# Optimization experiments

Measured on AMD Instinct MI355X. Metric: run time of the kernel, lower is better.

The kernel has to match this reference:

```python
import jax, jax.numpy as jnp
import numpy as np
from jax import lax

# dims from the TED skeleton used by speech2affective_gestures
N, T, J, C = 256, 1024, 9, 3      # batch, frames, directed edges (graph1 nodes), coords
K1, K2 = 5, 3                     # spatial partitions of A1, A2
F1, F2 = 16, 16                   # st_gcn output channels
NUM_PARTS, MAX_EDGES = 3, 3       # body parts, edges per part
BODY_PARTS = np.array([[0, 1, 2], [3, 4, 5], [6, 7, 8]])  # body_parts_edge_idx
EPS = 1e-5
LEAK = 0.01


def conv2d_nchw(x, w):
    kh = w.shape[2]
    return lax.conv_general_dilated(x, w, (1, 1), ((kh // 2, kh // 2), (0, 0)),
                                    dimension_numbers=("NCHW", "OIHW", "NCHW"))


def conv1d_nch(x, w):
    k = w.shape[2]
    return lax.conv_general_dilated(x, w, (1,), ((k // 2, k // 2),),
                                    dimension_numbers=("NCH", "OIH", "NCH"))


def bn1d(x, w, b, m, v):
    # inference-mode BatchNorm1d over channel axis 1 of (N, C, T)
    scale = w / jnp.sqrt(v + EPS)
    return x * scale[None, :, None] + (b - m * scale)[None, :, None]


def leaky(x):
    return jnp.where(x > 0, x, LEAK * x)


def setup_inputs() -> dict:
    key = jax.random.key(0)
    ks = jax.random.split(key, 12)
    s = 0.05
    return {
        "poses": jax.random.normal(ks[0], (N, T, J * C), jnp.float32),
        "A1": jax.random.uniform(ks[1], (K1, J, J), jnp.float32) / J,
        "A2": jax.random.uniform(ks[2], (K2, NUM_PARTS, NUM_PARTS), jnp.float32) / NUM_PARTS,
        "W1": jax.random.normal(ks[3], (F1 * K1, C, 9, 1), jnp.float32) * s,
        "b1": jnp.zeros((F1 * K1,), jnp.float32),
        "W2": jax.random.normal(ks[4], (F2 * K2, MAX_EDGES * F1, 9, 1), jnp.float32) * s,
        "b2": jnp.zeros((F2 * K2,), jnp.float32),
        "Wc1": jax.random.normal(ks[5], (16, F2 * NUM_PARTS, 5), jnp.float32) * s,
        "bc1": jnp.zeros((16,), jnp.float32),
        "bn1_w": jnp.ones((16,), jnp.float32), "bn1_b": jnp.zeros((16,), jnp.float32),
        "bn1_m": jnp.zeros((16,), jnp.float32), "bn1_v": jnp.ones((16,), jnp.float32),
        "Wc2": jax.random.normal(ks[6], (8, 16, 3), jnp.float32) * s,
        "bc2": jnp.zeros((8,), jnp.float32),
        "bn2_w": jnp.ones((8,), jnp.float32), "bn2_b": jnp.zeros((8,), jnp.float32),
        "bn2_m": jnp.zeros((8,), jnp.float32), "bn2_v": jnp.ones((8,), jnp.float32),
    }


def reference(poses, A1, A2, W1, b1, W2, b2, Wc1, bc1, bn1_w, bn1_b, bn1_m, bn1_v,
              Wc2, bc2, bn2_w, bn2_b, bn2_m, bn2_v):
    n, t, jc = poses.shape
    x = jnp.transpose(poses.reshape(n, t, J, C), (0, 3, 1, 2))  # (n, 3, t, 9)

    # st_gcn1: temporal conv -> split K partitions -> graph contraction with A1
    y = conv2d_nchw(x, W1) + b1[None, :, None, None]            # (n, K1*F1, t, 9)
    y = y.reshape(n, K1, F1, t, J)
    feat1 = jnp.einsum("nkctv,kvw->nctw", y, A1)                # (n, 16, t, 9)

    # body-part gather/pack: feat2_in channel layout is (c slow, edge fast)
    g = feat1[:, :, :, BODY_PARTS]                              # (n, 16, t, parts, edges)
    feat2_in = jnp.transpose(g, (0, 1, 4, 2, 3)).reshape(n, F1 * MAX_EDGES, t, NUM_PARTS)

    # st_gcn2
    y2 = conv2d_nchw(feat2_in, W2) + b2[None, :, None, None]    # (n, K2*F2, t, 3)
    y2 = y2.reshape(n, K2, F2, t, NUM_PARTS)
    feat2 = jnp.einsum("nkctv,kvw->nctw", y2, A2)               # (n, 16, t, 3)

    # flatten (c, v) with c slow -> (n, 48, t)
    feat3_in = jnp.transpose(feat2, (0, 1, 3, 2)).reshape(n, F2 * NUM_PARTS, t)

    h = leaky(bn1d(conv1d_nch(feat3_in, Wc1) + bc1[None, :, None], bn1_w, bn1_b, bn1_m, bn1_v))
    h = leaky(bn1d(conv1d_nch(h, Wc2) + bc2[None, :, None], bn2_w, bn2_b, bn2_m, bn2_v))
    return jnp.transpose(h, (0, 2, 1))                          # (n, t, 8)
```

## Files before the change

kernel.cpp:

```cpp
#include <hip/hip_runtime.h>

namespace {
constexpr int T_ = 1024;
constexpr int NBATCH = 256;

constexpr int WFB_OFF    = 0;
constexpr int WFC_OFF    = 82944;
constexpr int WFD_OFF    = 221184;
constexpr int WBIG_OFF   = 231424;
constexpr int WFE_OFF    = 252928;
constexpr int BIASB_OFF  = 254976;
constexpr int BIASC_OFF  = 255552;
constexpr int BIASD_OFF  = 255744;
constexpr int BIASBIG_OFF= 255808;
constexpr int BIASE_OFF  = 255872;

constexpr int R0 = 41472;
constexpr int R1 = R0 + 69120;
constexpr int R2 = R1 + 5120;
constexpr int R3 = R2 + 1024;
constexpr int R4 = R3 + 29952;
constexpr int R5 = R4 + 144;
constexpr int R6 = R5 + 48;
constexpr int R7 = R6 + 16;
constexpr int R8 = R7 + 8;

constexpr int SLAB_OFF  = 0;
constexpr int H1_OFF    = 18688;
constexpr int WBIGS_OFF = 27392;
constexpr int WFES_OFF  = 48896;
constexpr int SMEM_MAIN = 50944;
static_assert(SMEM_MAIN * 3 <= 163840, "3 blocks/CU");

constexpr int TT_FX     = 50;
constexpr int FXF2IN    = 0;
constexpr int FXF3      = FXF2IN + 72 * 320;
constexpr int FXSLAB    = FXF3 + 68 * 144;
constexpr int FXH1      = FXSLAB;
constexpr int SMEM_FX   = FXSLAB + 72 * 80;
static_assert(SMEM_FX <= 65536, "fixup LDS");

typedef __attribute__((ext_vector_type(8))) short short8v;
typedef __attribute__((ext_vector_type(4))) float f32x4;

__device__ inline unsigned short f2b(float f) {
  union { float f; unsigned u; } v; v.f = f;
  unsigned r = (v.u + 0x7FFFu + ((v.u >> 16) & 1u)) >> 16;
  return (unsigned short)r;
}
__device__ inline float b2f(unsigned short u) {
  union { unsigned u; float f; } v; v.u = ((unsigned)u) << 16;
  return v.f;
}
__device__ inline int fx_f2in_byte(int row, int slot, int within) {
  return FXF2IN + row * 320 + ((slot ^ ((row >> 2) & 3)) << 4) + within;
}
}

__global__ __launch_bounds__(256) void prep1_kernel(
    const float* __restrict__ A1, const float* __restrict__ A2,
    const float* __restrict__ W1, const float* __restrict__ b1,
    const float* __restrict__ W2, const float* __restrict__ b2,
    const float* __restrict__ Wc1, const float* __restrict__ bc1,
    const float* __restrict__ bn1w, const float* __restrict__ bn1b,
    const float* __restrict__ bn1m, const float* __restrict__ bn1v,
    const float* __restrict__ Wc2, const float* __restrict__ bc2,
    const float* __restrict__ bn2w, const float* __restrict__ bn2b,
    const float* __restrict__ bn2m, const float* __restrict__ bn2v,
    unsigned char* __restrict__ ws, float* __restrict__ wcomp) {
  unsigned short* wfB = (unsigned short*)(ws + WFB_OFF);
  unsigned short* wfC = (unsigned short*)(ws + WFC_OFF);
  unsigned short* wfD = (unsigned short*)(ws + WFD_OFF);
  unsigned short* wfE = (unsigned short*)(ws + WFE_OFF);
  float* biasB = (float*)(ws + BIASB_OFF);
  float* biasC = (float*)(ws + BIASC_OFF);
  float* biasD = (float*)(ws + BIASD_OFF);
  float* biasE = (float*)(ws + BIASE_OFF);
  for (int idx = blockIdx.x * 256 + threadIdx.x; idx < R8; idx += gridDim.x * 256) {
    if (idx < R0) {
      int ncol = idx / 288, k = idx - ncol * 288;
      int dh = k >> 5, mm = k & 31;
      float val = 0.f;
      if (mm < 27) {
        int v = mm / 3, ci = mm - v * 3;
        int p = ncol / 48, rr = ncol - p * 48, c = rr / 3, e = rr - c * 3;
        int w = p * 3 + e;
        for (int k5 = 0; k5 < 5; ++k5)
          val += W1[(k5 * 16 + c) * 27 + ci * 9 + dh] * A1[k5 * 81 + v * 9 + w];
      }
      wfB[idx] = f2b(val);
    } else if (idx < R1) {
      int i2 = idx - R0;
      int nc = i2 / 1440, k = i2 - nc * 1440;
      int dh = k / 160, off = k - dh * 160;
      float val = 0.f;
      if (off < 144) {
        int p = off / 48, ci2 = off - p * 48;
        int c2 = nc / 3, w2 = nc - c2 * 3;
        for (int k2 = 0; k2 < 3; ++k2)
          val += W2[(k2 * 16 + c2) * 432 + ci2 * 9 + dh] * A2[k2 * 9 + p * 3 + w2];
      }
      wfC[i2] = f2b(val);
    } else if (idx < R2) {
      int i3 = idx - R1;
      int o3 = i3 / 320, k = i3 - o3 * 320;
      int d = k >> 6, nc = k & 63;
      float val = 0.f;
      if (nc < 48) {
        float s1 = bn1w[o3] * rsqrtf(bn1v[o3] + 1e-5f);
        val = Wc1[o3 * 240 + nc * 5 + d] * s1;
      }
      wfD[i3] = f2b(val);
    } else if (idx < R3) {
      int i4 = idx - R2;
      int o4 = i4 >> 6, k = i4 & 63;
      float val = 0.f;
      if (o4 < 8 && k < 48) {
        int d = k >> 4, ci = k & 15;
        float s2 = bn2w[o4] * rsqrtf(bn2v[o4] + 1e-5f);
        val = Wc2[(o4 * 16 + ci) * 3 + d] * s2;
      }
      wfE[i4] = f2b(val);
    } else if (idx < R4) {
      int i5 = idx - R3;
      int o3 = i5 / 1872, rem = i5 - o3 * 1872;
      int dh2 = rem / 144, ncol = rem - dh2 * 144;
      int p = ncol / 48, ci2 = ncol - p * 48;
      float s1 = bn1w[o3] * rsqrtf(bn1v[o3] + 1e-5f);
      float acc = 0.f;
      for (int d = 0; d < 5; ++d) {
        int dh = dh2 - d;
        if (dh < 0 || dh > 8) continue;
        float wd = 0.f;
        for (int nc = 0; nc < 48; ++nc) {
          int c2 = nc / 3, w2 = nc - c2 * 3;
          float wc = 0.f;
          for (int k2 = 0; k2 < 3; ++k2)
            wc += W2[(k2 * 16 + c2) * 432 + ci2 * 9 + dh] * A2[k2 * 9 + p * 3 + w2];
          wd += Wc1[o3 * 240 + nc * 5 + d] * wc;
        }
        acc += wd * s1;
      }
      wcomp[i5] = acc;
    } else if (idx < R5) {
      int ib = idx - R4;
      int p = ib / 48, rr = ib - p * 48, c = rr / 3, e = rr - c * 3;
      int w = p * 3 + e;
      float val = 0.f;
      for (int k5 = 0; k5 < 5; ++k5)
        for (int v = 0; v < 9; ++v)
          val += b1[k5 * 16 + c] * A1[k5 * 81 + v * 9 + w];
      biasB[ib] = val;
    } else if (idx < R6) {
      int nc = idx - R5, c2 = nc / 3, w2 = nc - c2 * 3;
      float val = 0.f;
      for (int k2 = 0; k2 < 3; ++k2)
        for (int p = 0; p < 3; ++p)
          val += b2[k2 * 16 + c2] * A2[k2 * 9 + p * 3 + w2];
      biasC[nc] = val;
    } else if (idx < R7) {
      int o3 = idx - R6;
      float s1 = bn1w[o3] * rsqrtf(bn1v[o3] + 1e-5f);
      biasD[o3] = bc1[o3] * s1 + bn1b[o3] - bn1m[o3] * s1;
    } else {
      int o4 = idx - R7;
      float s2 = bn2w[o4] * rsqrtf(bn2v[o4] + 1e-5f);
      biasE[o4] = bc2[o4] * s2 + bn2b[o4] - bn2m[o4] * s2;
    }
  }
}

__global__ __launch_bounds__(256) void prep2_kernel(
    const float* __restrict__ Wc1, const float* __restrict__ bn1w,
    const float* __restrict__ bn1v, const float* __restrict__ wcomp,
    unsigned char* __restrict__ ws) {
  __shared__ float stgf[48 * 288];
  __shared__ float wl[1872];
  __shared__ float pr[256];
  __shared__ float pbias[192];
  const int dt = blockIdx.x, o3 = blockIdx.y;
  const int tid = threadIdx.x;
  const int m1 = tid & 31, p = tid >> 5;
  const unsigned short* wfB = (const unsigned short*)(ws + WFB_OFF);
  unsigned short* wBIG = (unsigned short*)(ws + WBIG_OFF);

  for (int i = tid; i < 1872; i += 256) wl[i] = wcomp[o3 * 1872 + i];

  const int lo = (dt - 8) > 0 ? (dt - 8) : 0;
  const int hi = (dt < 12) ? dt : 12;
  float acc = 0.f;
  for (int c = 0; c < 3; ++c) {
    __syncthreads();
    for (int i = tid; i < 48 * 288; i += 256)
      stgf[i] = b2f(wfB[c * 13824 + i]);
    __syncthreads();
    for (int dh2 = lo; dh2 <= hi; ++dh2) {
      const int dh1 = dt - dh2;
      const float* wr = wl + dh2 * 144 + c * 48 + p * 6;
      const float* br = stgf + (p * 6) * 288 + dh1 * 32 + m1;
#pragma unroll
      for (int j = 0; j < 6; ++j)
        acc += wr[j] * br[j * 288];
    }
  }
  pr[tid] = acc;
  __syncthreads();
  if (tid < 32) {
    float s = pr[tid];
#pragma unroll
    for (int pp = 1; pp < 8; ++pp) s += pr[pp * 32 + tid];
    wBIG[o3 * 672 + dt * 32 + tid] = f2b(s);
  }
  if (dt == 0) {
    if (tid < 144) {
      float s = 0.f;
      for (int dh2 = 0; dh2 < 13; ++dh2) s += wl[dh2 * 144 + tid];
      pbias[tid] = s * ((const float*)(ws + BIASB_OFF))[tid];
    } else if (tid < 192) {
      int nc = tid - 144;
      float s1 = bn1w[o3] * rsqrtf(bn1v[o3] + 1e-5f);
      float s = 0.f;
#pragma unroll
      for (int d = 0; d < 5; ++d) s += Wc1[o3 * 240 + nc * 5 + d];
      pbias[tid] = s * s1 * ((const float*)(ws + BIASC_OFF))[nc];
    }
    __syncthreads();
    if (tid == 0) {
      float accb = ((const float*)(ws + BIASD_OFF))[o3];
      for (int i = 0; i < 192; ++i) accb += pbias[i];
      ((float*)(ws + BIASBIG_OFF))[o3] = accb;
    }
  }
}

__global__ __launch_bounds__(256, 3) void main_kernel(
    const float* __restrict__ poses, const unsigned char* __restrict__ ws,
    float* __restrict__ out) {
  __shared__ __attribute__((aligned(16))) unsigned char smem[SMEM_MAIN];
  const int tid = threadIdx.x;
  const int n = blockIdx.y;
  const int t0 = blockIdx.x * 256;
  const int w = tid >> 6, l = tid & 63, lrow = l & 15, q = l >> 4, q8 = q * 8;

  {
    unsigned* s32 = (unsigned*)(smem + SLAB_OFF);
    for (int idx = tid; idx < 292 * 16; idx += 256) {
      int r = idx >> 4, mi = idx & 15, m0 = mi * 2;
      int t = t0 - 18 + r;
      float v0 = 0.f, v1 = 0.f;
      if (t >= 0 && t < T_) {
        const float* src = poses + ((long)n * T_ + t) * 27;
        if (m0 < 27) v0 = src[m0];
        if (m0 + 1 < 27) v1 = src[m0 + 1];
      }
      s32[idx] = (unsigned)f2b(v0) | ((unsigned)f2b(v1) << 16);
    }
    const unsigned* wbg = (const unsigned*)(ws + WBIG_OFF);
    unsigned* d1 = (unsigned*)(smem + WBIGS_OFF);
    for (int idx = tid; idx < 5376; idx += 256) d1[idx] = wbg[idx];
    const unsigned* wfe = (const unsigned*)(ws + WFE_OFF);
    unsigned* d2 = (unsigned*)(smem + WFES_OFF);
    for (int idx = tid; idx < 512; idx += 256) d2[idx] = wfe[idx];
  }
  __syncthreads();

  const float bb = ((const float*)(ws + BIASBIG_OFF))[lrow];
  const float be = ((const float*)(ws + BIASE_OFF))[lrow & 7];

  short8v B[21];
#pragma unroll
  for (int dt = 0; dt < 21; ++dt)
    B[dt] = *(const short8v*)(smem + WBIGS_OFF + lrow * 1344 + dt * 64 + q8 * 2);

#pragma unroll
  for (int i = 0; i < 5; ++i) {
    if (i == 4 && w != 0) continue;
    const int mt = (i < 4) ? (w + i * 4) : 16;
    const int sbase = SLAB_OFF + (mt * 16 + lrow) * 64 + q8 * 2;
    f32x4 c0 = {0.f, 0.f, 0.f, 0.f}, c1 = {0.f, 0.f, 0.f, 0.f};
    short8v a[7];
#pragma unroll
    for (int dt = 0; dt < 7; ++dt) a[dt] = *(const short8v*)(smem + sbase + dt * 64);
#pragma unroll
    for (int dt = 0; dt < 7; ++dt) {
      if (dt & 1) c1 = __builtin_amdgcn_mfma_f32_16x16x32_bf16(a[dt], B[dt], c1, 0, 0, 0);
      else        c0 = __builtin_amdgcn_mfma_f32_16x16x32_bf16(a[dt], B[dt], c0, 0, 0, 0);
    }
#pragma unroll
    for (int dt = 0; dt < 7; ++dt) a[dt] = *(const short8v*)(smem + sbase + (7 + dt) * 64);
#pragma unroll
    for (int dt = 0; dt < 7; ++dt) {
      if (dt & 1) c1 = __builtin_amdgcn_mfma_f32_16x16x32_bf16(a[dt], B[7 + dt], c1, 0, 0, 0);
      else        c0 = __builtin_amdgcn_mfma_f32_16x16x32_bf16(a[dt], B[7 + dt], c0, 0, 0, 0);
    }
#pragma unroll
    for (int dt = 0; dt < 7; ++dt) a[dt] = *(const short8v*)(smem + sbase + (14 + dt) * 64);
#pragma unroll
    for (int dt = 0; dt < 7; ++dt) {
      if (dt & 1) c1 = __builtin_amdgcn_mfma_f32_16x16x32_bf16(a[dt], B[14 + dt], c1, 0, 0, 0);
      else        c0 = __builtin_amdgcn_mfma_f32_16x16x32_bf16(a[dt], B[14 + dt], c0, 0, 0, 0);
    }
    const int hbase = H1_OFF + (mt * 16 + q * 4) * 32 + lrow * 2;
#pragma unroll
    for (int jj = 0; jj < 4; ++jj) {
      float x = c0[jj] + c1[jj] + bb;
      float h = x > 0.f ? x : 0.01f * x;
      *(unsigned short*)(smem + hbase + jj * 32) = f2b(h);
    }
  }
  __syncthreads();

  const short8v E0 = *(const short8v*)(smem + WFES_OFF + lrow * 128 + q8 * 2);
  const short8v E1 = *(const short8v*)(smem + WFES_OFF + lrow * 128 + 64 + q8 * 2);
#pragma unroll
  for (int i = 0; i < 4; ++i) {
    const int mte = w + i * 4;
    const int abase = H1_OFF + (7 + mte * 16 + lrow) * 32 + q8 * 2;
    short8v A0v = *(const short8v*)(smem + abase);
    short8v A1v = *(const short8v*)(smem + abase + 64);
    f32x4 acc = {0.f, 0.f, 0.f, 0.f};
    acc = __builtin_amdgcn_mfma_f32_16x16x32_bf16(A0v, E0, acc, 0, 0, 0);
    acc = __builtin_amdgcn_mfma_f32_16x16x32_bf16(A1v, E1, acc, 0, 0, 0);
    if (lrow < 8) {
      const long ob = ((long)n * T_ + t0 + mte * 16 + q * 4) * 8 + lrow;
#pragma unroll
      for (int jj = 0; jj < 4; ++jj) {
        float x = acc[jj] + be;
        out[ob + jj * 8] = x > 0.f ? x : 0.01f * x;
      }
    }
  }
}

__global__ __launch_bounds__(256, 4) void fixup_kernel(
    const float* __restrict__ poses,
    const float* __restrict__ Wc2, const float* __restrict__ bc2,
    const float* __restrict__ bn2w, const float* __restrict__ bn2b,
    const float* __restrict__ bn2m, const float* __restrict__ bn2v,
    const unsigned char* __restrict__ ws, float* __restrict__ out) {
  __shared__ __attribute__((aligned(16))) unsigned char smem[SMEM_FX];
  const unsigned short* wfB = (const unsigned short*)(ws + WFB_OFF);
  const unsigned short* wfC = (const unsigned short*)(ws + WFC_OFF);
  const unsigned short* wfD = (const unsigned short*)(ws + WFD_OFF);
  const float* biasB = (const float*)(ws + BIASB_OFF);
  const float* biasC = (const float*)(ws + BIASC_OFF);
  const float* biasD = (const float*)(ws + BIASD_OFF);

  const int tid = threadIdx.x;
  const int n = blockIdx.y;
  const int e = blockIdx.x;
  const int t0 = e ? (T_ - TT_FX) : 0;
  const int w = tid >> 6;
  const int l = tid & 63;
  const int lrow = l & 15;
  const int q = l >> 4;
  const int q8 = q * 8;

  {
    unsigned* slab32 = (unsigned*)(smem + FXSLAB);
    for (int it = tid; it < 72 * 20; it += 256) {
      int r = it / 20, mi = it - r * 20;
      int t = t0 - 11 + r;
      int m0 = mi * 2;
      float v0 = 0.f, v1 = 0.f;
      if (t >= 0 && t < T_) {
        const float* src = poses + ((long)n * T_ + t) * 27;
        if (m0 < 27) v0 = src[m0];
        if (m0 + 1 < 27) v1 = src[m0 + 1];
      }
      slab32[it] = (unsigned)f2b(v0) | ((unsigned)f2b(v1) << 16);
    }
    for (int it = tid; it < 64 * 8; it += 256) {
      int r = it >> 3, u = it & 7;
      int s = 18 + (u >> 2);
      *(unsigned*)(smem + fx_f2in_byte(r, s, (u & 3) * 4)) = 0;
    }
    for (int it = tid; it < 8 * 80; it += 256) {
      int r = 64 + it / 80, u = it - (it / 80) * 80;
      *(unsigned*)(smem + FXF2IN + r * 320 + u * 4) = 0;
    }
    for (int it = tid; it < 68 * 8 + 12 * 24; it += 256) {
      if (it < 68 * 8) {
        int r = it >> 3, u = it & 7;
        *(unsigned*)(smem + FXF3 + r * 144 + 96 + u * 4) = 0;
      } else {
        int k2 = it - 68 * 8;
        int r = 56 + k2 / 24, u = k2 - (k2 / 24) * 24;
        *(unsigned*)(smem + FXF3 + r * 144 + u * 4) = 0;
      }
    }
  }
  __syncthreads();

  {
    const int ntS = (w == 0) ? 0 : (2 * w + 1);
    const int ntN = (w == 0) ? 3 : 2;
#pragma unroll
    for (int ni = 0; ni < 3; ++ni) {
      if (ni < ntN) {
        const int nt = ntS + ni;
        short8v b[9];
#pragma unroll
        for (int dh = 0; dh < 9; ++dh)
          b[dh] = *(const short8v*)(wfB + (nt * 16 + lrow) * 288 + dh * 32 + q8);
        const int ncol = nt * 16 + lrow;
        const float bias = biasB[ncol];
#pragma unroll
        for (int mt = 0; mt < 4; ++mt) {
          short8v a[9];
#pragma unroll
          for (int dh = 0; dh < 9; ++dh)
            a[dh] = *(const short8v*)(smem + FXSLAB + ((mt * 16 + lrow + dh) * 40 + q8) * 2);
          f32x4 c0 = {0.f, 0.f, 0.f, 0.f}, c1 = {0.f, 0.f, 0.f, 0.f};
#pragma unroll
          for (int dh = 0; dh < 9; ++dh) {
            if (dh & 1) c1 = __builtin_amdgcn_mfma_f32_16x16x32_bf16(a[dh], b[dh], c1, 0, 0, 0);
            else        c0 = __builtin_amdgcn_mfma_f32_16x16x32_bf16(a[dh], b[dh], c0, 0, 0, 0);
          }
#pragma unroll
          for (int jj = 0; jj < 4; ++jj) {
            const int r = mt * 16 + q * 4 + jj;
            const int t = t0 - 7 + r;
            float v = (t >= 0 && t < T_) ? c0[jj] + c1[jj] + bias : 0.f;
            *(unsigned short*)(smem + fx_f2in_byte(r, ncol >> 3, (ncol & 7) * 2)) = f2b(v);
          }
        }
      }
    }
  }
  __syncthreads();

  if (w < 3) {
    const int nt = w;
    const int ncol2 = nt * 16 + lrow;
    const float bias = biasC[ncol2];
    f32x4 acc[4];
#pragma unroll
    for (int mt = 0; mt < 4; ++mt) acc[mt] = {0.f, 0.f, 0.f, 0.f};
#pragma unroll
    for (int g = 0; g < 5; ++g) {
      short8v b[9];
#pragma unroll
      for (int i = 0; i < 9; ++i) {
        const int kf = g * 9 + i, dh = kf / 5, kkl = kf % 5;
        b[i] = *(const short8v*)(wfC + ncol2 * 1440 + dh * 160 + kkl * 32 + q8);
      }
#pragma unroll
      for (int mt = 0; mt < 4; ++mt) {
        short8v a[9];
#pragma unroll
        for (int i = 0; i < 9; ++i) {
          const int kf = g * 9 + i, dh = kf / 5, kkl = kf % 5;
          a[i] = *(const short8v*)(smem + fx_f2in_byte(mt * 16 + lrow + dh, 4 * kkl + q, 0));
        }
#pragma unroll
        for (int i = 0; i < 9; ++i)
          acc[mt] = __builtin_amdgcn_mfma_f32_16x16x32_bf16(a[i], b[i], acc[mt], 0, 0, 0);
      }
    }
#pragma unroll
    for (int mt = 0; mt < 4; ++mt) {
#pragma unroll
      for (int jj = 0; jj < 4; ++jj) {
        const int rt3 = mt * 16 + q * 4 + jj;
        if (rt3 < 56) {
          const int t = t0 - 3 + rt3;
          float v = (t >= 0 && t < T_) ? acc[mt][jj] + bias : 0.f;
          *(unsigned short*)(smem + FXF3 + rt3 * 144 + ncol2 * 2) = f2b(v);
        }
      }
    }
  }
  __syncthreads();

  {
    const int arow = w * 16 + lrow;
    short8v a[10], b[10];
#pragma unroll
    for (int kf = 0; kf < 10; ++kf) {
      const int d = kf >> 1, kkl = kf & 1;
      b[kf] = *(const short8v*)(wfD + lrow * 320 + d * 64 + kkl * 32 + q8);
      a[kf] = *(const short8v*)(smem + FXF3 + (arow + d) * 144 + (kkl * 32 + q8) * 2);
    }
    f32x4 c0 = {0.f, 0.f, 0.f, 0.f}, c1 = {0.f, 0.f, 0.f, 0.f};
#pragma unroll
    for (int kf = 0; kf < 10; ++kf) {
      if (kf & 1) c1 = __builtin_amdgcn_mfma_f32_16x16x32_bf16(a[kf], b[kf], c1, 0, 0, 0);
      else        c0 = __builtin_amdgcn_mfma_f32_16x16x32_bf16(a[kf], b[kf], c0, 0, 0, 0);
    }
    const float bias = biasD[lrow];
#pragma unroll
    for (int jj = 0; jj < 4; ++jj) {
      const int rh = w * 16 + q * 4 + jj;
      if (rh < 52) {
        const int t = t0 - 1 + rh;
        float v = 0.f;
        if (t >= 0 && t < T_) {
          float x = c0[jj] + c1[jj] + bias;
          v = x > 0.f ? x : 0.01f * x;
        }
        *(float*)(smem + FXH1 + (rh * 17 + lrow) * 4) = v;
      }
    }
  }
  __syncthreads();

  for (int it = tid; it < TT_FX * 8; it += 256) {
    int rt = it >> 3, o4 = it & 7;
    int t = t0 + rt;
    if (t >= T_) continue;
    if (e ? (t < 1017) : (t >= 7)) continue;
    float s2 = bn2w[o4] * rsqrtf(bn2v[o4] + 1e-5f);
    float t2 = bc2[o4] * s2 + bn2b[o4] - bn2m[o4] * s2;
    float acc = 0.f;
#pragma unroll
    for (int d = 0; d < 3; ++d) {
      const float* hr = (const float*)(smem + FXH1 + (rt + d) * 68);
#pragma unroll
      for (int ci = 0; ci < 16; ++ci)
        acc = fmaf(hr[ci], Wc2[(o4 * 16 + ci) * 3 + d], acc);
    }
    float v = acc * s2 + t2;
    out[((long)n * T_ + t) * 8 + o4] = v > 0.f ? v : 0.01f * v;
  }
}

extern "C" void kernel_launch(void* const* d_in, const int* in_sizes, int n_in,
                              void* d_out, int out_size, void* d_ws, size_t ws_size,
                              hipStream_t stream) {
  (void)in_sizes; (void)n_in; (void)out_size; (void)ws_size;
  const float* poses = (const float*)d_in[0];
  const float* A1    = (const float*)d_in[1];
  const float* A2    = (const float*)d_in[2];
  const float* W1    = (const float*)d_in[3];
  const float* b1    = (const float*)d_in[4];
  const float* W2    = (const float*)d_in[5];
  const float* b2    = (const float*)d_in[6];
  const float* Wc1   = (const float*)d_in[7];
  const float* bc1   = (const float*)d_in[8];
  const float* bn1w  = (const float*)d_in[9];
  const float* bn1b  = (const float*)d_in[10];
  const float* bn1m  = (const float*)d_in[11];
  const float* bn1v  = (const float*)d_in[12];
  const float* Wc2   = (const float*)d_in[13];
  const float* bc2   = (const float*)d_in[14];
  const float* bn2w  = (const float*)d_in[15];
  const float* bn2b  = (const float*)d_in[16];
  const float* bn2m  = (const float*)d_in[17];
  const float* bn2v  = (const float*)d_in[18];
  float* out = (float*)d_out;
  unsigned char* ws = (unsigned char*)d_ws;
  float* wcomp = (float*)d_out;

  hipLaunchKernelGGL(prep1_kernel, dim3(144), dim3(256), 0, stream,
                     A1, A2, W1, b1, W2, b2, Wc1, bc1, bn1w, bn1b, bn1m, bn1v,
                     Wc2, bc2, bn2w, bn2b, bn2m, bn2v, ws, wcomp);
  hipLaunchKernelGGL(prep2_kernel, dim3(21, 16), dim3(256), 0, stream,
                     Wc1, bn1w, bn1v, wcomp, ws);
  hipLaunchKernelGGL(main_kernel, dim3(4, NBATCH), dim3(256), 0, stream,
                     poses, ws, out);
  hipLaunchKernelGGL(fixup_kernel, dim3(2, NBATCH), dim3(256), 0, stream,
                     poses, Wc2, bc2, bn2w, bn2b, bn2m, bn2v, ws, out);
}
```

Measured before the change: 87.44 us.

## Merge prep kernels and fuse main and fixup into one launch

Merges the two weight-preparation kernels into one launch: the extra blocks build the composed conv2+conv3 weights in LDS, per output channel, without going through a global scratch buffer. The main and edge-fixup kernels become one kernel using blockIdx.x to choose the path. The main path now reads the composed weights straight from global memory into registers instead of staging them in LDS, and skips writing edge timesteps that the fixup blocks produce. This cuts launches from four to two and removes the read-after-write ordering between main and fixup. In exchange, the per-channel composition runs serially on only 16 blocks.

```diff
diff --git a/kernel.cpp b/kernel.cpp
--- a/kernel.cpp
+++ b/kernel.cpp
@@ -15,30 +15,25 @@
 constexpr int BIASBIG_OFF= 255808;
 constexpr int BIASE_OFF  = 255872;
 
-constexpr int R0 = 41472;
-constexpr int R1 = R0 + 69120;
-constexpr int R2 = R1 + 5120;
-constexpr int R3 = R2 + 1024;
-constexpr int R4 = R3 + 29952;
-constexpr int R5 = R4 + 144;
-constexpr int R6 = R5 + 48;
-constexpr int R7 = R6 + 16;
-constexpr int R8 = R7 + 8;
+constexpr int S0 = 41472;
+constexpr int S1 = S0 + 69120;
+constexpr int S2 = S1 + 5120;
+constexpr int S3 = S2 + 1024;
+constexpr int S4 = S3 + 144;
+constexpr int S5 = S4 + 48;
+constexpr int S6 = S5 + 16;
+constexpr int S7 = S6 + 8;
+constexpr int NPREP = 115;
 
 constexpr int SLAB_OFF  = 0;
 constexpr int H1_OFF    = 18688;
-constexpr int WBIGS_OFF = 27392;
-constexpr int WFES_OFF  = 48896;
-constexpr int SMEM_MAIN = 50944;
-static_assert(SMEM_MAIN * 3 <= 163840, "3 blocks/CU");
-
 constexpr int TT_FX     = 50;
 constexpr int FXF2IN    = 0;
 constexpr int FXF3      = FXF2IN + 72 * 320;
 constexpr int FXSLAB    = FXF3 + 68 * 144;
 constexpr int FXH1      = FXSLAB;
-constexpr int SMEM_FX   = FXSLAB + 72 * 80;
-static_assert(SMEM_FX <= 65536, "fixup LDS");
+constexpr int SMEM_FUSE = FXSLAB + 72 * 80;
+static_assert(SMEM_FUSE <= 65536, "fused LDS");
 
 typedef __attribute__((ext_vector_type(8))) short short8v;
 typedef __attribute__((ext_vector_type(4))) float f32x4;
@@ -57,7 +52,7 @@
 }
 }
 
-__global__ __launch_bounds__(256) void prep1_kernel(
+__global__ __launch_bounds__(256) void prep_kernel(
     const float* __restrict__ A1, const float* __restrict__ A2,
     const float* __restrict__ W1, const float* __restrict__ b1,
     const float* __restrict__ W2, const float* __restrict__ b2,
@@ -67,294 +62,308 @@
     const float* __restrict__ Wc2, const float* __restrict__ bc2,
     const float* __restrict__ bn2w, const float* __restrict__ bn2b,
     const float* __restrict__ bn2m, const float* __restrict__ bn2v,
-    unsigned char* __restrict__ ws, float* __restrict__ wcomp) {
-  unsigned short* wfB = (unsigned short*)(ws + WFB_OFF);
-  unsigned short* wfC = (unsigned short*)(ws + WFC_OFF);
-  unsigned short* wfD = (unsigned short*)(ws + WFD_OFF);
-  unsigned short* wfE = (unsigned short*)(ws + WFE_OFF);
-  float* biasB = (float*)(ws + BIASB_OFF);
-  float* biasC = (float*)(ws + BIASC_OFF);
-  float* biasD = (float*)(ws + BIASD_OFF);
-  float* biasE = (float*)(ws + BIASE_OFF);
-  for (int idx = blockIdx.x * 256 + threadIdx.x; idx < R8; idx += gridDim.x * 256) {
-    if (idx < R0) {
-      int ncol = idx / 288, k = idx - ncol * 288;
-      int dh = k >> 5, mm = k & 31;
-      float val = 0.f;
-      if (mm < 27) {
-        int v = mm / 3, ci = mm - v * 3;
-        int p = ncol / 48, rr = ncol - p * 48, c = rr / 3, e = rr - c * 3;
+    unsigned char* __restrict__ ws) {
+  __shared__ float wcl[13 * 144];
+  __shared__ float slice[48 * 144];
+  __shared__ float pb[192];
+  const int tid = threadIdx.x;
+
+  if (blockIdx.x < NPREP) {
+    unsigned short* wfB = (unsigned short*)(ws + WFB_OFF);
+    unsigned short* wfC = (unsigned short*)(ws + WFC_OFF);
+    unsigned short* wfD = (unsigned short*)(ws + WFD_OFF);
+    unsigned short* wfE = (unsigned short*)(ws + WFE_OFF);
+    float* biasB = (float*)(ws + BIASB_OFF);
+    float* biasC = (float*)(ws + BIASC_OFF);
+    float* biasD = (float*)(ws + BIASD_OFF);
+    float* biasE = (float*)(ws + BIASE_OFF);
+    for (int idx = blockIdx.x * 256 + tid; idx < S7; idx += NPREP * 256) {
+      if (idx < S0) {
+        int ncol = idx / 288, k = idx - ncol * 288;
+        int dh = k >> 5, mm = k & 31;
+        float val = 0.f;
+        if (mm < 27) {
+          int v = mm / 3, ci = mm - v * 3;
+          int p = ncol / 48, rr = ncol - p * 48, c = rr / 3, e = rr - c * 3;
+          int w = p * 3 + e;
+          for (int k5 = 0; k5 < 5; ++k5)
+            val += W1[(k5 * 16 + c) * 27 + ci * 9 + dh] * A1[k5 * 81 + v * 9 + w];
+        }
+        wfB[idx] = f2b(val);
+      } else if (idx < S1) {
+        int i2 = idx - S0;
+        int nc = i2 / 1440, k = i2 - nc * 1440;
+        int dh = k / 160, off = k - dh * 160;
+        float val = 0.f;
+        if (off < 144) {
+          int p = off / 48, ci2 = off - p * 48;
+          int c2 = nc / 3, w2 = nc - c2 * 3;
+          for (int k2 = 0; k2 < 3; ++k2)
+            val += W2[(k2 * 16 + c2) * 432 + ci2 * 9 + dh] * A2[k2 * 9 + p * 3 + w2];
+        }
+        wfC[i2] = f2b(val);
+      } else if (idx < S2) {
+        int i3 = idx - S1;
+        int o3 = i3 / 320, k = i3 - o3 * 320;
+        int d = k >> 6, nc = k & 63;
+        float val = 0.f;
+        if (nc < 48) {
+          float s1 = bn1w[o3] * rsqrtf(bn1v[o3] + 1e-5f);
+          val = Wc1[o3 * 240 + nc * 5 + d] * s1;
+        }
+        wfD[i3] = f2b(val);
+      } else if (idx < S3) {
+        int i4 = idx - S2;
+        int o4 = i4 >> 6, k = i4 & 63;
+        float val = 0.f;
+        if (o4 < 8 && k < 48) {
+          int d = k >> 4, ci = k & 15;
+          float s2 = bn2w[o4] * rsqrtf(bn2v[o4] + 1e-5f);
+          val = Wc2[(o4 * 16 + ci) * 3 + d] * s2;
+        }
+        wfE[i4] = f2b(val);
+      } else if (idx < S4) {
+        int ib = idx - S3;
+        int p = ib / 48, rr = ib - p * 48, c = rr / 3, e = rr - c * 3;
         int w = p * 3 + e;
+        float val = 0.f;
         for (int k5 = 0; k5 < 5; ++k5)
-          val += W1[(k5 * 16 + c) * 27 + ci * 9 + dh] * A1[k5 * 81 + v * 9 + w];
-      }
-      wfB[idx] = f2b(val);
-    } else if (idx < R1) {
-      int i2 = idx - R0;
-      int nc = i2 / 1440, k = i2 - nc * 1440;
-      int dh = k / 160, off = k - dh * 160;
-      float val = 0.f;
-      if (off < 144) {
-        int p = off / 48, ci2 = off - p * 48;
-        int c2 = nc / 3, w2 = nc - c2 * 3;
+          for (int v = 0; v < 9; ++v)
+            val += b1[k5 * 16 + c] * A1[k5 * 81 + v * 9 + w];
+        biasB[ib] = val;
+      } else if (idx < S5) {
+        int nc = idx - S4, c2 = nc / 3, w2 = nc - c2 * 3;
+        float val = 0.f;
         for (int k2 = 0; k2 < 3; ++k2)
-          val += W2[(k2 * 16 + c2) * 432 + ci2 * 9 + dh] * A2[k2 * 9 + p * 3 + w2];
-      }
-      wfC[i2] = f2b(val);
-    } else if (idx < R2) {
-      int i3 = idx - R1;
-      int o3 = i3 / 320, k = i3 - o3 * 320;
-      int d = k >> 6, nc = k & 63;
-      float val = 0.f;
-      if (nc < 48) {
+          for (int p = 0; p < 3; ++p)
+            val += b2[k2 * 16 + c2] * A2[k2 * 9 + p * 3 + w2];
+        biasC[nc] = val;
+      } else if (idx < S6) {
+        int o3 = idx - S5;
         float s1 = bn1w[o3] * rsqrtf(bn1v[o3] + 1e-5f);
-        val = Wc1[o3 * 240 + nc * 5 + d] * s1;
-      }
-      wfD[i3] = f2b(val);
-    } else if (idx < R3) {
-      int i4 = idx - R2;
-      int o4 = i4 >> 6, k = i4 & 63;
-      float val = 0.f;
-      if (o4 < 8 && k < 48) {
-        int d = k >> 4, ci = k & 15;
+        biasD[o3] = bc1[o3] * s1 + bn1b[o3] - bn1m[o3] * s1;
+      } else {
+        int o4 = idx - S6;
         float s2 = bn2w[o4] * rsqrtf(bn2v[o4] + 1e-5f);
-        val = Wc2[(o4 * 16 + ci) * 3 + d] * s2;
-      }
-      wfE[i4] = f2b(val);
-    } else if (idx < R4) {
-      int i5 = idx - R3;
-      int o3 = i5 / 1872, rem = i5 - o3 * 1872;
-      int dh2 = rem / 144, ncol = rem - dh2 * 144;
+        biasE[o4] = bc2[o4] * s2 + bn2b[o4] - bn2m[o4] * s2;
+      }
+    }
+    return;
+  }
+
+  const int o3 = blockIdx.x - NPREP;
+  const float s1 = bn1w[o3] * rsqrtf(bn1v[o3] + 1e-5f);
+  unsigned short* wBIG = (unsigned short*)(ws + WBIG_OFF);
+
+  for (int i = tid; i < 1872; i += 256) wcl[i] = 0.f;
+  __syncthreads();
+  for (int dh = 0; dh < 9; ++dh) {
+    for (int i = tid; i < 6912; i += 256) {
+      int nc = i / 144, ncol = i - nc * 144;
       int p = ncol / 48, ci2 = ncol - p * 48;
-      float s1 = bn1w[o3] * rsqrtf(bn1v[o3] + 1e-5f);
-      float acc = 0.f;
+      int c2 = nc / 3, w2 = nc - c2 * 3;
+      float v = 0.f;
+      for (int k2 = 0; k2 < 3; ++k2)
+        v += W2[(k2 * 16 + c2) * 432 + ci2 * 9 + dh] * A2[k2 * 9 + p * 3 + w2];
+      slice[i] = v;
+    }
+    __syncthreads();
+    if (tid < 144) {
+#pragma unroll
       for (int d = 0; d < 5; ++d) {
-        int dh = dh2 - d;
-        if (dh < 0 || dh > 8) continue;
-        float wd = 0.f;
-        for (int nc = 0; nc < 48; ++nc) {
-          int c2 = nc / 3, w2 = nc - c2 * 3;
-          float wc = 0.f;
-          for (int k2 = 0; k2 < 3; ++k2)
-            wc += W2[(k2 * 16 + c2) * 432 + ci2 * 9 + dh] * A2[k2 * 9 + p * 3 + w2];
-          wd += Wc1[o3 * 240 + nc * 5 + d] * wc;
-        }
-        acc += wd * s1;
-      }
-      wcomp[i5] = acc;
-    } else if (idx < R5) {
-      int ib = idx - R4;
-      int p = ib / 48, rr = ib - p * 48, c = rr / 3, e = rr - c * 3;
+        float wv = 0.f;
+        for (int nc = 0; nc < 48; ++nc)
+          wv += Wc1[o3 * 240 + nc * 5 + d] * slice[nc * 144 + tid];
+        wcl[(dh + d) * 144 + tid] += wv * s1;
+      }
+    }
+    __syncthreads();
+  }
+
+  float acc0 = 0.f, acc1 = 0.f, acc2 = 0.f;
+  const int sl0 = tid, sl1 = tid + 256, sl2 = tid + 512;
+  for (int dh1 = 0; dh1 < 9; ++dh1) {
+    for (int i = tid; i < 3888; i += 256) {
+      int ncol = i / 27, m = i - ncol * 27;
+      int vv = m / 3, ci = m - vv * 3;
+      int p = ncol / 48, rr = ncol - p * 48, c = rr / 3, e = rr - c * 3;
       int w = p * 3 + e;
       float val = 0.f;
       for (int k5 = 0; k5 < 5; ++k5)
-        for (int v = 0; v < 9; ++v)
-          val += b1[k5 * 16 + c] * A1[k5 * 81 + v * 9 + w];
-      biasB[ib] = val;
-    } else if (idx < R6) {
-      int nc = idx - R5, c2 = nc / 3, w2 = nc - c2 * 3;
-      float val = 0.f;
-      for (int k2 = 0; k2 < 3; ++k2)
-        for (int p = 0; p < 3; ++p)
-          val += b2[k2 * 16 + c2] * A2[k2 * 9 + p * 3 + w2];
-      biasC[nc] = val;
-    } else if (idx < R7) {
-      int o3 = idx - R6;
-      float s1 = bn1w[o3] * rsqrtf(bn1v[o3] + 1e-5f);
-      biasD[o3] = bc1[o3] * s1 + bn1b[o3] - bn1m[o3] * s1;
-    } else {
-      int o4 = idx - R7;
-      float s2 = bn2w[o4] * rsqrtf(bn2v[o4] + 1e-5f);
-      biasE[o4] = bc2[o4] * s2 + bn2b[o4] - bn2m[o4] * s2;
-    }
-  }
-}
-
-__global__ __launch_bounds__(256) void prep2_kernel(
-    const float* __restrict__ Wc1, const float* __restrict__ bn1w,
-    const float* __restrict__ bn1v, const float* __restrict__ wcomp,
-    unsigned char* __restrict__ ws) {
-  __shared__ float stgf[48 * 288];
-  __shared__ float wl[1872];
-  __shared__ float pr[256];
-  __shared__ float pbias[192];
-  const int dt = blockIdx.x, o3 = blockIdx.y;
-  const int tid = threadIdx.x;
-  const int m1 = tid & 31, p = tid >> 5;
-  const unsigned short* wfB = (const unsigned short*)(ws + WFB_OFF);
-  unsigned short* wBIG = (unsigned short*)(ws + WBIG_OFF);
-
-  for (int i = tid; i < 1872; i += 256) wl[i] = wcomp[o3 * 1872 + i];
-
-  const int lo = (dt - 8) > 0 ? (dt - 8) : 0;
-  const int hi = (dt < 12) ? dt : 12;
-  float acc = 0.f;
-  for (int c = 0; c < 3; ++c) {
+        val += W1[(k5 * 16 + c) * 27 + ci * 9 + dh1] * A1[k5 * 81 + vv * 9 + w];
+      slice[i] = val;
+    }
     __syncthreads();
-    for (int i = tid; i < 48 * 288; i += 256)
-      stgf[i] = b2f(wfB[c * 13824 + i]);
+    {
+      int dt = sl0 >> 5, mm = sl0 & 31, dh2 = dt - dh1;
+      if (mm < 27 && dh2 >= 0 && dh2 <= 12)
+        for (int ncol = 0; ncol < 144; ++ncol)
+          acc0 += wcl[dh2 * 144 + ncol] * slice[ncol * 27 + mm];
+    }
+    {
+      int dt = sl1 >> 5, mm = sl1 & 31, dh2 = dt - dh1;
+      if (mm < 27 && dh2 >= 0 && dh2 <= 12)
+        for (int ncol = 0; ncol < 144; ++ncol)
+          acc1 += wcl[dh2 * 144 + ncol] * slice[ncol * 27 + mm];
+    }
+    if (sl2 < 672) {
+      int dt = sl2 >> 5, mm = sl2 & 31, dh2 = dt - dh1;
+      if (mm < 27 && dh2 >= 0 && dh2 <= 12)
+        for (int ncol = 0; ncol < 144; ++ncol)
+          acc2 += wcl[dh2 * 144 + ncol] * slice[ncol * 27 + mm];
+    }
     __syncthreads();
-    for (int dh2 = lo; dh2 <= hi; ++dh2) {
-      const int dh1 = dt - dh2;
-      const float* wr = wl + dh2 * 144 + c * 48 + p * 6;
-      const float* br = stgf + (p * 6) * 288 + dh1 * 32 + m1;
-#pragma unroll
-      for (int j = 0; j < 6; ++j)
-        acc += wr[j] * br[j * 288];
-    }
-  }
-  pr[tid] = acc;
-  __syncthreads();
-  if (tid < 32) {
-    float s = pr[tid];
-#pragma unroll
-    for (int pp = 1; pp < 8; ++pp) s += pr[pp * 32 + tid];
-    wBIG[o3 * 672 + dt * 32 + tid] = f2b(s);
-  }
-  if (dt == 0) {
-    if (tid < 144) {
-      float s = 0.f;
-      for (int dh2 = 0; dh2 < 13; ++dh2) s += wl[dh2 * 144 + tid];
-      pbias[tid] = s * ((const float*)(ws + BIASB_OFF))[tid];
-    } else if (tid < 192) {
-      int nc = tid - 144;
-      float s1 = bn1w[o3] * rsqrtf(bn1v[o3] + 1e-5f);
-      float s = 0.f;
-#pragma unroll
-      for (int d = 0; d < 5; ++d) s += Wc1[o3 * 240 + nc * 5 + d];
-      pbias[tid] = s * s1 * ((const float*)(ws + BIASC_OFF))[nc];
-    }
-    __syncthreads();
-    if (tid == 0) {
-      float accb = ((const float*)(ws + BIASD_OFF))[o3];
-      for (int i = 0; i < 192; ++i) accb += pbias[i];
-      ((float*)(ws + BIASBIG_OFF))[o3] = accb;
-    }
-  }
-}
-
-__global__ __launch_bounds__(256, 3) void main_kernel(
-    const float* __restrict__ poses, const unsigned char* __restrict__ ws,
-    float* __restrict__ out) {
-  __shared__ __attribute__((aligned(16))) unsigned char smem[SMEM_MAIN];
-  const int tid = threadIdx.x;
-  const int n = blockIdx.y;
-  const int t0 = blockIdx.x * 256;
-  const int w = tid >> 6, l = tid & 63, lrow = l & 15, q = l >> 4, q8 = q * 8;
-
-  {
-    unsigned* s32 = (unsigned*)(smem + SLAB_OFF);
-    for (int idx = tid; idx < 292 * 16; idx += 256) {
-      int r = idx >> 4, mi = idx & 15, m0 = mi * 2;
-      int t = t0 - 18 + r;
-      float v0 = 0.f, v1 = 0.f;
-      if (t >= 0 && t < T_) {
-        const float* src = poses + ((long)n * T_ + t) * 27;
-        if (m0 < 27) v0 = src[m0];
-        if (m0 + 1 < 27) v1 = src[m0 + 1];
-      }
-      s32[idx] = (unsigned)f2b(v0) | ((unsigned)f2b(v1) << 16);
-    }
-    const unsigned* wbg = (const unsigned*)(ws + WBIG_OFF);
-    unsigned* d1 = (unsigned*)(smem + WBIGS_OFF);
-    for (int idx = tid; idx < 5376; idx += 256) d1[idx] = wbg[idx];
-    const unsigned* wfe = (const unsigned*)(ws + WFE_OFF);
-    unsigned* d2 = (unsigned*)(smem + WFES_OFF);
-    for (int idx = tid; idx < 512; idx += 256) d2[idx] = wfe[idx];
-  }
-  __syncthreads();
-
-  const float bb = ((const float*)(ws + BIASBIG_OFF))[lrow];
-  const float be = ((const float*)(ws + BIASE_OFF))[lrow & 7];
-
-  short8v B[21];
-#pragma unroll
-  for (int dt = 0; dt < 21; ++dt)
-    B[dt] = *(const short8v*)(smem + WBIGS_OFF + lrow * 1344 + dt * 64 + q8 * 2);
-
-#pragma unroll
-  for (int i = 0; i < 5; ++i) {
-    if (i == 4 && w != 0) continue;
-    const int mt = (i < 4) ? (w + i * 4) : 16;
-    const int sbase = SLAB_OFF + (mt * 16 + lrow) * 64 + q8 * 2;
-    f32x4 c0 = {0.f, 0.f, 0.f, 0.f}, c1 = {0.f, 0.f, 0.f, 0.f};
-    short8v a[7];
-#pragma unroll
-    for (int dt = 0; dt < 7; ++dt) a[dt] = *(const short8v*)(smem + sbase + dt * 64);
-#pragma unroll
-    for (int dt = 0; dt < 7; ++dt) {
-      if (dt & 1) c1 = __builtin_amdgcn_mfma_f32_16x16x32_bf16(a[dt], B[dt], c1, 0, 0, 0);
-      else        c0 = __builtin_amdgcn_mfma_f32_16x16x32_bf16(a[dt], B[dt], c0, 0, 0, 0);
-    }
-#pragma unroll
-    for (int dt = 0; dt < 7; ++dt) a[dt] = *(const short8v*)(smem + sbase + (7 + dt) * 64);
-#pragma unroll
-    for (int dt = 0; dt < 7; ++dt) {
-      if (dt & 1) c1 = __builtin_amdgcn_mfma_f32_16x16x32_bf16(a[dt], B[7 + dt], c1, 0, 0, 0);
-      else        c0 = __builtin_amdgcn_mfma_f32_16x16x32_bf16(a[dt], B[7 + dt], c0, 0, 0, 0);
-    }
-#pragma unroll
-    for (int dt = 0; dt < 7; ++dt) a[dt] = *(const short8v*)(smem + sbase + (14 + dt) * 64);
-#pragma unroll
-    for (int dt = 0; dt < 7; ++dt) {
-      if (dt & 1) c1 = __builtin_amdgcn_mfma_f32_16x16x32_bf16(a[dt], B[14 + dt], c1, 0, 0, 0);
-      else        c0 = __builtin_amdgcn_mfma_f32_16x16x32_bf16(a[dt], B[14 + dt], c0, 0, 0, 0);
-    }
-    const int hbase = H1_OFF + (mt * 16 + q * 4) * 32 + lrow * 2;
-#pragma unroll
-    for (int jj = 0; jj < 4; ++jj) {
-      float x = c0[jj] + c1[jj] + bb;
-      float h = x > 0.f ? x : 0.01f * x;
-      *(unsigned short*)(smem + hbase + jj * 32) = f2b(h);
-    }
-  }
-  __syncthreads();
-
-  const short8v E0 = *(const short8v*)(smem + WFES_OFF + lrow * 128 + q8 * 2);
-  const short8v E1 = *(const short8v*)(smem + WFES_OFF + lrow * 128 + 64 + q8 * 2);
-#pragma unroll
-  for (int i = 0; i < 4; ++i) {
-    const int mte = w + i * 4;
-    const int abase = H1_OFF + (7 + mte * 16 + lrow) * 32 + q8 * 2;
-    short8v A0v = *(const short8v*)(smem + abase);
-    short8v A1v = *(const short8v*)(smem + abase + 64);
-    f32x4 acc = {0.f, 0.f, 0.f, 0.f};
-    acc = __builtin_amdgcn_mfma_f32_16x16x32_bf16(A0v, E0, acc, 0, 0, 0);
-    acc = __builtin_amdgcn_mfma_f32_16x16x32_bf16(A1v, E1, acc, 0, 0, 0);
-    if (lrow < 8) {
-      const long ob = ((long)n * T_ + t0 + mte * 16 + q * 4) * 8 + lrow;
-#pragma unroll
-      for (int jj = 0; jj < 4; ++jj) {
-        float x = acc[jj] + be;
-        out[ob + jj * 8] = x > 0.f ? x : 0.01f * x;
-      }
-    }
-  }
-}
-
-__global__ __launch_bounds__(256, 4) void fixup_kernel(
+  }
+  wBIG[o3 * 672 + sl0] = f2b(((sl0 & 31) < 27) ? acc0 : 0.f);
+  wBIG[o3 * 672 + sl1] = f2b(((sl1 & 31) < 27) ? acc1 : 0.f);
+  if (sl2 < 672) wBIG[o3 * 672 + sl2] = f2b(((sl2 & 31) < 27) ? acc2 : 0.f);
+
+  if (tid < 144) {
+    int p = tid / 48, rr = tid - p * 48, c = rr / 3, e = rr - c * 3;
+    int w = p * 3 + e;
+    float val = 0.f;
+    for (int k5 = 0; k5 < 5; ++k5)
+      for (int v = 0; v < 9; ++v)
+        val += b1[k5 * 16 + c] * A1[k5 * 81 + v * 9 + w];
+    pb[tid] = val;
+  } else if (tid < 192) {
+    int nc = tid - 144, c2 = nc / 3, w2 = nc - c2 * 3;
+    float val = 0.f;
+    for (int k2 = 0; k2 < 3; ++k2)
+      for (int p = 0; p < 3; ++p)
+        val += b2[k2 * 16 + c2] * A2[k2 * 9 + p * 3 + w2];
+    pb[tid] = val;
+  }
+  __syncthreads();
+  if (tid < 144) {
+    float s = 0.f;
+    for (int dh2 = 0; dh2 < 13; ++dh2) s += wcl[dh2 * 144 + tid];
+    slice[tid] = s * pb[tid];
+  } else if (tid < 192) {
+    int nc = tid - 144;
+    float s = 0.f;
+#pragma unroll
+    for (int d = 0; d < 5; ++d) s += Wc1[o3 * 240 + nc * 5 + d];
+    slice[tid] = s * s1 * pb[tid];
+  }
+  __syncthreads();
+  if (tid == 0) {
+    float accb = bc1[o3] * s1 + bn1b[o3] - bn1m[o3] * s1;
+    for (int i = 0; i < 192; ++i) accb += slice[i];
+    ((float*)(ws + BIASBIG_OFF))[o3] = accb;
+  }
+}
+
+__global__ __launch_bounds__(256, 3) void fused_kernel(
     const float* __restrict__ poses,
     const float* __restrict__ Wc2, const float* __restrict__ bc2,
     const float* __restrict__ bn2w, const float* __restrict__ bn2b,
     const float* __restrict__ bn2m, const float* __restrict__ bn2v,
     const unsigned char* __restrict__ ws, float* __restrict__ out) {
-  __shared__ __attribute__((aligned(16))) unsigned char smem[SMEM_FX];
+  __shared__ __attribute__((aligned(16))) unsigned char smem[SMEM_FUSE];
+  const int tid = threadIdx.x;
+  const int n = blockIdx.y;
+  const int w = tid >> 6, l = tid & 63, lrow = l & 15, q = l >> 4, q8 = q * 8;
+
+  if (blockIdx.x < 4) {
+    const int t0 = blockIdx.x * 256;
+    {
+      unsigned* s32 = (unsigned*)(smem + SLAB_OFF);
+      for (int idx = tid; idx < 292 * 16; idx += 256) {
+        int r = idx >> 4, mi = idx & 15, m0 = mi * 2;
+        int t = t0 - 18 + r;
+        float v0 = 0.f, v1 = 0.f;
+        if (t >= 0 && t < T_) {
+          const float* src = poses + ((long)n * T_ + t) * 27;
+          if (m0 < 27) v0 = src[m0];
+          if (m0 + 1 < 27) v1 = src[m0 + 1];
+        }
+        s32[idx] = (unsigned)f2b(v0) | ((unsigned)f2b(v1) << 16);
+      }
+    }
+
+    const float bb = ((const float*)(ws + BIASBIG_OFF))[lrow];
+    const float be = ((const float*)(ws + BIASE_OFF))[lrow & 7];
+    const unsigned short* wbg = (const unsigned short*)(ws + WBIG_OFF);
+    short8v B[21];
+#pragma unroll
+    for (int dt = 0; dt < 21; ++dt)
+      B[dt] = *(const short8v*)(wbg + lrow * 672 + dt * 32 + q8);
+    const unsigned short* wfe = (const unsigned short*)(ws + WFE_OFF);
+    const short8v E0 = *(const short8v*)(wfe + lrow * 64 + q8);
+    const short8v E1 = *(const short8v*)(wfe + lrow * 64 + 32 + q8);
+    __syncthreads();
+
+#pragma unroll
+    for (int i = 0; i < 5; ++i) {
+      if (i == 4 && w != 0) continue;
+      const int mt = (i < 4) ? (w + i * 4) : 16;
+      const int sbase = SLAB_OFF + (mt * 16 + lrow) * 64 + q8 * 2;
+      f32x4 c0 = {0.f, 0.f, 0.f, 0.f}, c1 = {0.f, 0.f, 0.f, 0.f};
+      short8v a[7];
+#pragma unroll
+      for (int dt = 0; dt < 7; ++dt) a[dt] = *(const short8v*)(smem + sbase + dt * 64);
+#pragma unroll
+      for (int dt = 0; dt < 7; ++dt) {
+        if (dt & 1) c1 = __builtin_amdgcn_mfma_f32_16x16x32_bf16(a[dt], B[dt], c1, 0, 0, 0);
+        else        c0 = __builtin_amdgcn_mfma_f32_16x16x32_bf16(a[dt], B[dt], c0, 0, 0, 0);
+      }
+#pragma unroll
+      for (int dt = 0; dt < 7; ++dt) a[dt] = *(const short8v*)(smem + sbase + (7 + dt) * 64);
+#pragma unroll
+      for (int dt = 0; dt < 7; ++dt) {
+        if (dt & 1) c1 = __builtin_amdgcn_mfma_f32_16x16x32_bf16(a[dt], B[7 + dt], c1, 0, 0, 0);
+        else        c0 = __builtin_amdgcn_mfma_f32_16x16x32_bf16(a[dt], B[7 + dt], c0, 0, 0, 0);
+      }
+#pragma unroll
+      for (int dt = 0; dt < 7; ++dt) a[dt] = *(const short8v*)(smem + sbase + (14 + dt) * 64);
+#pragma unroll
+      for (int dt = 0; dt < 7; ++dt) {
+        if (dt & 1) c1 = __builtin_amdgcn_mfma_f32_16x16x32_bf16(a[dt], B[14 + dt], c1, 0, 0, 0);
+        else        c0 = __builtin_amdgcn_mfma_f32_16x16x32_bf16(a[dt], B[14 + dt], c0, 0, 0, 0);
+      }
+      const int hbase = H1_OFF + (mt * 16 + q * 4) * 32 + lrow * 2;
+#pragma unroll
+      for (int jj = 0; jj < 4; ++jj) {
+        float x = c0[jj] + c1[jj] + bb;
+        float h = x > 0.f ? x : 0.01f * x;
+        *(unsigned short*)(smem + hbase + jj * 32) = f2b(h);
+      }
+    }
+    __syncthreads();
+
+#pragma unroll
+    for (int i = 0; i < 4; ++i) {
+      const int mte = w + i * 4;
+      const int abase = H1_OFF + (7 + mte * 16 + lrow) * 32 + q8 * 2;
+      short8v A0v = *(const short8v*)(smem + abase);
+      short8v A1v = *(const short8v*)(smem + abase + 64);
+      f32x4 acc = {0.f, 0.f, 0.f, 0.f};
+      acc = __builtin_amdgcn_mfma_f32_16x16x32_bf16(A0v, E0, acc, 0, 0, 0);
+      acc = __builtin_amdgcn_mfma_f32_16x16x32_bf16(A1v, E1, acc, 0, 0, 0);
+      if (lrow < 8) {
+        const int tb = t0 + mte * 16 + q * 4;
+#pragma unroll
+        for (int jj = 0; jj < 4; ++jj) {
+          const int t = tb + jj;
+          if (t >= 7 && t < 1017) {
+            float x = acc[jj] + be;
+            out[((long)n * T_ + t) * 8 + lrow] = x > 0.f ? x : 0.01f * x;
+          }
+        }
+      }
+    }
+    return;
+  }
+
   const unsigned short* wfB = (const unsigned short*)(ws + WFB_OFF);
   const unsigned short* wfC = (const unsigned short*)(ws + WFC_OFF);
   const unsigned short* wfD = (const unsigned short*)(ws + WFD_OFF);
   const float* biasB = (const float*)(ws + BIASB_OFF);
   const float* biasC = (const float*)(ws + BIASC_OFF);
   const float* biasD = (const float*)(ws + BIASD_OFF);
-
-  const int tid = threadIdx.x;
-  const int n = blockIdx.y;
-  const int e = blockIdx.x;
+  const int e = blockIdx.x - 4;
   const int t0 = e ? (T_ - TT_FX) : 0;
-  const int w = tid >> 6;
-  const int l = tid & 63;
-  const int lrow = l & 15;
-  const int q = l >> 4;
-  const int q8 = q * 8;
 
   {
     unsigned* slab32 = (unsigned*)(smem + FXSLAB);
@@ -431,8 +440,7 @@
   __syncthreads();
 
   if (w < 3) {
-    const int nt = w;
-    const int ncol2 = nt * 16 + lrow;
+    const int ncol2 = w * 16 + lrow;
     const float bias = biasC[ncol2];
     f32x4 acc[4];
 #pragma unroll
@@ -550,15 +558,10 @@
   const float* bn2v  = (const float*)d_in[18];
   float* out = (float*)d_out;
   unsigned char* ws = (unsigned char*)d_ws;
-  float* wcomp = (float*)d_out;
-
-  hipLaunchKernelGGL(prep1_kernel, dim3(144), dim3(256), 0, stream,
+
+  hipLaunchKernelGGL(prep_kernel, dim3(NPREP + 16), dim3(256), 0, stream,
                      A1, A2, W1, b1, W2, b2, Wc1, bc1, bn1w, bn1b, bn1m, bn1v,
-                     Wc2, bc2, bn2w, bn2b, bn2m, bn2v, ws, wcomp);
-  hipLaunchKernelGGL(prep2_kernel, dim3(21, 16), dim3(256), 0, stream,
-                     Wc1, bn1w, bn1v, wcomp, ws);
-  hipLaunchKernelGGL(main_kernel, dim3(4, NBATCH), dim3(256), 0, stream,
-                     poses, ws, out);
-  hipLaunchKernelGGL(fixup_kernel, dim3(2, NBATCH), dim3(256), 0, stream,
+                     Wc2, bc2, bn2w, bn2b, bn2m, bn2v, ws);
+  hipLaunchKernelGGL(fused_kernel, dim3(6, NBATCH), dim3(256), 0, stream,
                      poses, Wc2, bc2, bn2w, bn2b, bn2m, bn2v, ws, out);
 }
```

Measured after the change: 167.9 us. 92.1% more time.
